# Performance work log

Hardware: AMD Instinct MI355X
Metric: run time of the kernel (lower is better)

Reference implementation:

```python
import jax, jax.numpy as jnp
import numpy as np

V, EMB, H, N, E, B = 100000, 300, 64, 20000, 160000, 4096
L, T = 2, 3  # layer_timesteps = [3, 3]


def setup_inputs() -> dict:
    key = jax.random.key(0)
    ks = jax.random.split(key, 24)
    ri = lambda k, shape, hi: jax.random.randint(k, shape, 0, hi)
    rn = lambda k, shape, s=0.05: (jax.random.normal(k, shape, dtype=jnp.float32) * s)
    emb_table = rn(ks[7], (V, EMB), 0.1).at[0].set(0.0)  # padding_idx=0 row is zeros
    return {
        'emb_ind0': ri(ks[0], (N,), V),
        'emb_ind1': ri(ks[1], (N,), V),
        'adj0': ri(ks[2], (E, 2), N),
        'adj1': ri(ks[3], (E, 2), N),
        'prop_ind0': ri(ks[4], (B,), N),
        'prop_ind1': ri(ks[5], (B,), N),
        'labels': ri(ks[6], (B,), 2),
        'emb_table': emb_table,
        'proj_W': rn(ks[8], (EMB, H)),   # emb_proj weight (stored input-major)
        'proj_b': jnp.zeros((H,), jnp.float32),
        'msg_W': rn(ks[9], (L, H, H)),   # per-layer edge-type-0 message linear
        'msg_b': jnp.zeros((L, H), jnp.float32),
        'gru_Wih': rn(ks[10], (L, 3 * H, H)),
        'gru_Whh': rn(ks[11], (L, 3 * H, H)),
        'gru_bih': jnp.zeros((L, 3 * H), jnp.float32),
        'gru_bhh': jnp.zeros((L, 3 * H), jnp.float32),
        'cla_W1': rn(ks[12], (2 * H, 16)),
        'cla_b1': jnp.zeros((16,), jnp.float32),
        'cla_W2': rn(ks[13], (16, 1)),
        'cla_b2': jnp.zeros((1,), jnp.float32),
    }


def _gru_cell(x, h, Wih, Whh, bih, bhh):
    # torch.nn.GRUCell math
    gi = x @ Wih.T + bih
    gh = h @ Whh.T + bhh
    i_r, i_z, i_n = jnp.split(gi, 3, axis=-1)
    h_r, h_z, h_n = jnp.split(gh, 3, axis=-1)
    r = jax.nn.sigmoid(i_r + h_r)
    z = jax.nn.sigmoid(i_z + h_z)
    n = jnp.tanh(i_n + r * h_n)
    return (1.0 - z) * n + z * h


def reference(emb_ind0, emb_ind1, adj0, adj1, prop_ind0, prop_ind1, labels,
              emb_table, proj_W, proj_b, msg_W, msg_b,
              gru_Wih, gru_Whh, gru_bih, gru_bhh,
              cla_W1, cla_b1, cla_W2, cla_b2):
    def ggnn(x, adj):
        src, tgt = adj[:, 0], adj[:, 1]
        h = x
        for l in range(L):              # 2 structurally distinct layers
            for _ in range(T):          # 3 timesteps each
                m = h[src] @ msg_W[l] + msg_b[l]                     # [E, H] gather + transform
                inc = jax.ops.segment_sum(m, tgt, num_segments=N)    # scatter-add messages
                h = _gru_cell(inc, h, gru_Wih[l], gru_Whh[l], gru_bih[l], gru_bhh[l])
        return h

    def branch(emb_ind, adj, prop_ind):
        ge = emb_table[emb_ind]          # embedding lookup [N, EMB]
        ge = ge @ proj_W + proj_b        # emb_proj -> [N, H]
        ge = ggnn(ge, adj)
        return ge[prop_ind]              # index_select -> [B, H]

    g0 = branch(emb_ind0, adj0, prop_ind0)
    g1 = branch(emb_ind1, adj1, prop_ind1)
    ge = jnp.concatenate([g0, g1], axis=-1)                 # match='concat' -> [B, 2H]
    hid = jax.nn.relu(ge @ cla_W1 + cla_b1)
    logits = jax.nn.sigmoid(hid @ cla_W2 + cla_b2)          # [B, 1], num_class=1 path
    p = logits.squeeze(-1)
    y = labels.astype(p.dtype)
    eps = 1e-7  # mirrors torch BCELoss log-clamping
    loss = -jnp.mean(y * jnp.log(jnp.clip(p, eps, 1.0))
                     + (1.0 - y) * jnp.log(jnp.clip(1.0 - p, eps, 1.0)))
    return logits, loss
```

## Files before the change

### kernel.cpp

```cpp
#include <hip/hip_runtime.h>
#include <hip/hip_bf16.h>

typedef unsigned short u16;
typedef __attribute__((ext_vector_type(8))) short s16x8;
typedef __attribute__((ext_vector_type(4))) float f32x4;

#define NN 20000
#define HH 64
#define EMBD 300
#define EE 160000
#define BB 4096
#define NODES 40000

#define PROJM_REP 7

#define OFF_PROJB 0
#define OFF_MSGB  64
#define OFF_BIH   192
#define OFF_BHH   576
#define OFF_CW1T  960
#define OFF_CB1   3008
#define OFF_CW2   3024
#define OFF_CB2   3040
#define PARAM_SZ  3072

#define PB_WIH   0
#define PB_WHH   24576
#define PB_WMT   49152
#define PB_PROJT 57344
#define PB_SZ    77824

#define APAD 344

#define ZCNT (16 + 2 * (NN + 1))

__device__ __forceinline__ float b2f(u16 u) {
    union { unsigned int i; float f; } v; v.i = ((unsigned int)u) << 16; return v.f;
}
__device__ __forceinline__ u16 f2b(float f) {
    union { float f; unsigned int u; } v; v.f = f;
    unsigned int u = v.u;
    return (u16)((u + 0x7FFFu + ((u >> 16) & 1u)) >> 16);
}
__device__ __forceinline__ float ldf(const void* p, long long i, int isbf) {
    return isbf ? b2f(((const u16*)p)[i]) : ((const float*)p)[i];
}
__device__ __forceinline__ u16 ldb(const void* p, long long i, int isbf) {
    return isbf ? ((const u16*)p)[i] : f2b(((const float*)p)[i]);
}
__device__ __forceinline__ void stf(void* p, long long i, int isbf, float v) {
    if (isbf) ((u16*)p)[i] = f2b(v);
    else      ((float*)p)[i] = v;
}

__device__ __forceinline__ int sniff_inline(const u16* probe, int tid)
{
    u16 x = probe[2 * (tid & 63)];
    unsigned int e = (x >> 7) & 0xFF;
    unsigned long long m = __ballot(e >= 105 && e <= 127);
    return (__popcll(m) >= 48) ? 1 : 0;
}

__global__ __launch_bounds__(256) void conv_kernel(
    const void* projW, const void* projb, const void* msgW, const void* msgb,
    const void* wih, const void* whh, const void* bih, const void* bhh,
    const void* cw1, const void* cb1, const void* cw2, const void* cb2,
    float* P, u16* PB, int* zbase)
{
    int tid = threadIdx.x;
    int isbf = sniff_inline((const u16*)projW, tid);
    int i = blockIdx.x * 256 + tid;

    if (i < ZCNT) zbase[i] = 0;

    if (i < 64)    P[OFF_PROJB + i] = ldf(projb, i, isbf);
    if (i < 128)   P[OFF_MSGB + i]  = ldf(msgb, i, isbf);
    if (i < 384)   { P[OFF_BIH + i] = ldf(bih, i, isbf); P[OFF_BHH + i] = ldf(bhh, i, isbf); }
    if (i < 2048)  { int t = i >> 7, k = i & 127; P[OFF_CW1T + i] = ldf(cw1, (long long)k * 16 + t, isbf); }
    if (i < 16)    { P[OFF_CB1 + i] = ldf(cb1, i, isbf); P[OFF_CW2 + i] = ldf(cw2, i, isbf); }
    if (i == 0)    P[OFF_CB2] = ldf(cb2, 0, isbf);

    if (i < 24576) {
        int l = i / 12288, r = i - l * 12288;
        int frag = r >> 9, rr = r & 511, lane = rr >> 3, e = rr & 7;
        int jt = frag >> 1, kt = frag & 1;
        int srow = jt * 16 + (lane & 15);
        int sk = kt * 32 + ((lane >> 4) << 3) + e;
        long long si = (long long)l * 12288 + srow * 64 + sk;
        PB[PB_WIH + i] = ldb(wih, si, isbf);
        PB[PB_WHH + i] = ldb(whh, si, isbf);
    }
    if (i < 8192) {
        int l = i >> 12, r = i & 4095;
        int frag = r >> 9, rr = r & 511, lane = rr >> 3, e = rr & 7;
        int jt = frag >> 1, kt = frag & 1;
        int srow = jt * 16 + (lane & 15);
        int sk = kt * 32 + ((lane >> 4) << 3) + e;
        PB[PB_WMT + i] = ldb(msgW, (long long)l * 4096 + sk * 64 + srow, isbf);
    }
    if (i < 20480) {
        int frag = i >> 9, rr = i & 511, lane = rr >> 3, e = rr & 7;
        int jt = frag / 10, kt = frag - jt * 10;
        int srow = jt * 16 + (lane & 15);
        int sk = kt * 32 + ((lane >> 4) << 3) + e;
        PB[PB_PROJT + i] = (sk < 300) ? ldb(projW, (long long)sk * 64 + srow, isbf) : (u16)0;
    }
}

__global__ __launch_bounds__(256) void hist_kernel(const int* __restrict__ adj0,
                                                   const int* __restrict__ adj1, int* off)
{
    int e = blockIdx.x * 256 + threadIdx.x;
    if (e >= 2 * EE) return;
    int b = e / EE, le = e - b * EE;
    const int* adj = b ? adj1 : adj0;
    int tgt = adj[2 * le + 1];
    atomicAdd(&off[b * (NN + 1) + tgt + 1], 1);
}

__global__ __launch_bounds__(1024) void scan_kernel(int* off, int* cursor)
{
    int b = blockIdx.x;
    int* o = off + (size_t)b * (NN + 1);
    int* cur = cursor + (size_t)b * NN;
    __shared__ int wsum[16];
    __shared__ int wscan[16];
    int tid = threadIdx.x, wv = tid >> 6, lane = tid & 63;

    int vpre[20];
    #pragma unroll
    for (int c = 0; c < 20; ++c) {
        int i = c * 1024 + tid;
        vpre[c] = (i < NN) ? o[i + 1] : 0;
    }

    int base = 0;
    #pragma unroll 1
    for (int c = 0; c < 20; ++c) {
        int i = c * 1024 + tid;
        int v = vpre[c];
        int orig = v;
        #pragma unroll
        for (int d = 1; d < 64; d <<= 1) {
            int t = __shfl_up(v, d);
            if (lane >= d) v += t;
        }
        if (lane == 63) wsum[wv] = v;
        __syncthreads();
        if (tid < 16) {
            int w = wsum[tid];
            #pragma unroll
            for (int d = 1; d < 16; d <<= 1) {
                int t = __shfl_up(w, d, 16);
                if (tid >= d) w += t;
            }
            wscan[tid] = w;
        }
        __syncthreads();
        int woff = (wv == 0) ? 0 : wscan[wv - 1];
        int excl = base + woff + v - orig;
        if (i < NN) { o[i] = excl; cur[i] = excl; }
        base += wscan[15];
    }
    if (tid == 0) o[NN] = base;
}

__global__ __launch_bounds__(256) void scatter_kernel(const int* __restrict__ adj0,
                                                      const int* __restrict__ adj1,
                                                      int* cursor, int* esrc)
{
    int e = blockIdx.x * 256 + threadIdx.x;
    if (e >= 2 * EE) return;
    int b = e / EE, le = e - b * EE;
    const int* adj = b ? adj1 : adj0;
    int src = adj[2 * le + 0];
    int tgt = adj[2 * le + 1];
    int pos = atomicAdd(&cursor[b * NN + tgt], 1);
    esrc[(size_t)b * EE + pos] = src;
}

__global__ __launch_bounds__(256) void projm_kernel(const void* emb,
                                                    const int* __restrict__ i0,
                                                    const int* __restrict__ i1,
                                                    const float* __restrict__ P,
                                                    const u16* __restrict__ PB,
                                                    u16* __restrict__ h,
                                                    const u16* __restrict__ probe)
{
    __shared__ u16 sA[64 * APAD];
    int tid = threadIdx.x;
    int isbf = sniff_inline(probe, tid);
    int node0 = blockIdx.x * 64;

    #pragma unroll 1
    for (int rep = 0; rep < PROJM_REP; ++rep) {
        {
            int r = tid >> 2, sub = tid & 3;
            int n = node0 + r;
            int b = n >= NN;
            int ln = n - b * NN;
            int idx = b ? i1[ln] : i0[ln];
            if (isbf) {
                const ushort4* src = (const ushort4*)((const u16*)emb + (size_t)idx * EMBD);
                ushort4* dst = (ushort4*)(sA + r * APAD);
                for (int c = sub; c < 75; c += 4) dst[c] = src[c];
                if (sub == 0) {
                    ushort4 z = {0, 0, 0, 0};
                    for (int c = 75; c < 80; ++c) dst[c] = z;
                }
            } else {
                const float4* src = (const float4*)((const float*)emb + (size_t)idx * EMBD);
                ushort4* dst = (ushort4*)(sA + r * APAD);
                for (int c = sub; c < 75; c += 4) {
                    float4 f = src[c];
                    ushort4 o4 = { f2b(f.x), f2b(f.y), f2b(f.z), f2b(f.w) };
                    dst[c] = o4;
                }
                if (sub == 0) {
                    ushort4 z = {0, 0, 0, 0};
                    for (int c = 75; c < 80; ++c) dst[c] = z;
                }
            }
        }

        int wv = tid >> 6, lane = tid & 63, quad = lane >> 4, cn = lane & 15;
        int m0 = wv * 16;
        f32x4 acc[4];
        #pragma unroll
        for (int j = 0; j < 4; ++j) {
            float bb = P[OFF_PROJB + j * 16 + cn];
            acc[j] = {bb, bb, bb, bb};
        }
        #pragma unroll
        for (int kt = 0; kt < 10; ++kt) {
            s16x8 a = *(const s16x8*)&sA[(m0 + cn) * APAD + kt * 32 + quad * 8];
            #pragma unroll
            for (int j = 0; j < 4; ++j) {
                s16x8 bfr = *(const s16x8*)&PB[PB_PROJT + (j * 10 + kt) * 512 + lane * 8];
                acc[j] = __builtin_amdgcn_mfma_f32_16x16x32_bf16(a, bfr, acc[j], 0, 0, 0);
            }
        }
        #pragma unroll
        for (int j = 0; j < 4; ++j)
            #pragma unroll
            for (int r = 0; r < 4; ++r)
                h[(size_t)(node0 + m0 + quad * 4 + r) * 64 + j * 16 + cn] = f2b(acc[j][r]);
    }
}

__global__ __launch_bounds__(256) void fstep_kernel(const u16* __restrict__ h_old,
                                                    u16* __restrict__ h_new,
                                                    const int* __restrict__ ioff,
                                                    const int* __restrict__ esrc,
                                                    const float* __restrict__ P,
                                                    const u16* __restrict__ PB, int l)
{
    __shared__ u16 s_S[32 * 64];
    __shared__ u16 s_h[32 * 64];
    __shared__ float s_deg[32];

    int tid = threadIdx.x;
    int bsw = blockIdx.x;
    int half = (bsw >> 2) & 1;
    int t = (bsw >> 3) * 4 + (bsw & 3);
    if (t >= 625) return;
    int node0 = half * NN + t * 32;

    {
        int team = tid >> 3, oct = tid & 7;
        int node = node0 + team;
        int br = node >= NN;
        int ln = node - br * NN;
        const int* o = ioff + (size_t)br * (NN + 1);
        int s0 = o[ln], s1 = o[ln + 1];
        const int* es = esrc + (size_t)br * EE;
        const u16* hb = h_old + (size_t)br * NN * 64;

        *(uint4*)&s_h[team * 64 + oct * 8] =
            *(const uint4*)&h_old[(size_t)node * 64 + oct * 8];
        if (oct == 0) s_deg[team] = (float)(s1 - s0);

        float acc[8];
        #pragma unroll
        for (int k = 0; k < 8; ++k) acc[k] = 0.f;

        int base = s0, rem = s1 - s0;
        while (rem > 0) {
            int cnt = rem < 8 ? rem : 8;
            int myidx = es[base + (oct < cnt ? oct : cnt - 1)];
            #pragma unroll
            for (int j = 0; j < 8; ++j) {
                int e = __shfl(myidx, j, 8);
                uint4 v = *(const uint4*)&hb[(size_t)e * 64 + oct * 8];
                float w = (j < cnt) ? 1.f : 0.f;
                #pragma unroll
                for (int p = 0; p < 4; ++p) {
                    unsigned int u = ((const unsigned int*)&v)[p];
                    union { unsigned int i; float f; } lo, hi;
                    lo.i = u << 16; hi.i = u & 0xffff0000u;
                    acc[2 * p]     += w * lo.f;
                    acc[2 * p + 1] += w * hi.f;
                }
            }
            base += cnt;
            rem -= cnt;
        }

        u16 pk[8];
        #pragma unroll
        for (int k = 0; k < 8; ++k) pk[k] = f2b(acc[k]);
        *(uint4*)&s_S[team * 64 + oct * 8] = *(const uint4*)pk;
    }
    __syncthreads();

    int wv = tid >> 6, lane = tid & 63;
    int wr = wv >> 1, wc = wv & 1;
    int m0 = wr * 16;
    int quad = lane >> 4, cn = lane & 15;
    int arow = (m0 + cn) * 64 + quad * 8;
    int fl = lane * 8;

    s16x8 aS0 = *(const s16x8*)&s_S[arow];
    s16x8 aS1 = *(const s16x8*)&s_S[arow + 32];
    s16x8 aH0 = *(const s16x8*)&s_h[arow];
    s16x8 aH1 = *(const s16x8*)&s_h[arow + 32];
    __syncthreads();

    const u16* WM = PB + PB_WMT + (size_t)l * 4096;
    #pragma unroll
    for (int jtl = 0; jtl < 2; ++jtl) {
        int jt = wc * 2 + jtl;
        float mb = P[OFF_MSGB + l * 64 + jt * 16 + cn];
        f32x4 acc;
        acc[0] = s_deg[m0 + quad * 4 + 0] * mb;
        acc[1] = s_deg[m0 + quad * 4 + 1] * mb;
        acc[2] = s_deg[m0 + quad * 4 + 2] * mb;
        acc[3] = s_deg[m0 + quad * 4 + 3] * mb;
        acc = __builtin_amdgcn_mfma_f32_16x16x32_bf16(aS0, *(const s16x8*)&WM[(jt * 2 + 0) * 512 + fl], acc, 0, 0, 0);
        acc = __builtin_amdgcn_mfma_f32_16x16x32_bf16(aS1, *(const s16x8*)&WM[(jt * 2 + 1) * 512 + fl], acc, 0, 0, 0);
        #pragma unroll
        for (int r = 0; r < 4; ++r)
            s_S[(m0 + quad * 4 + r) * 64 + jt * 16 + cn] = f2b(acc[r]);
    }
    __syncthreads();

    s16x8 aI0 = *(const s16x8*)&s_S[arow];
    s16x8 aI1 = *(const s16x8*)&s_S[arow + 32];
    __syncthreads();

    const u16* WI = PB + PB_WIH + (size_t)l * 12288;
    const u16* WH = PB + PB_WHH + (size_t)l * 12288;
    const float* bi = P + OFF_BIH + l * 192;
    const float* bh = P + OFF_BHH + l * 192;

    #pragma unroll
    for (int cl = 0; cl < 2; ++cl) {
        int jt = wc * 2 + cl;
        int j0 = jt * 16;
        float vr = bi[j0 + cn], vz = bi[64 + j0 + cn], vn = bi[128 + j0 + cn];
        float wr_ = bh[j0 + cn], wz = bh[64 + j0 + cn], wn = bh[128 + j0 + cn];
        f32x4 gr = {vr, vr, vr, vr}, gz = {vz, vz, vz, vz}, gn = {vn, vn, vn, vn};
        f32x4 hr = {wr_, wr_, wr_, wr_}, hz = {wz, wz, wz, wz}, hn = {wn, wn, wn, wn};
        int fr = (jt * 2) * 512 + fl, frz = ((4 + jt) * 2) * 512 + fl, frn = ((8 + jt) * 2) * 512 + fl;
        gr = __builtin_amdgcn_mfma_f32_16x16x32_bf16(aI0, *(const s16x8*)&WI[fr], gr, 0, 0, 0);
        gr = __builtin_amdgcn_mfma_f32_16x16x32_bf16(aI1, *(const s16x8*)&WI[fr + 512], gr, 0, 0, 0);
        gz = __builtin_amdgcn_mfma_f32_16x16x32_bf16(aI0, *(const s16x8*)&WI[frz], gz, 0, 0, 0);
        gz = __builtin_amdgcn_mfma_f32_16x16x32_bf16(aI1, *(const s16x8*)&WI[frz + 512], gz, 0, 0, 0);
        gn = __builtin_amdgcn_mfma_f32_16x16x32_bf16(aI0, *(const s16x8*)&WI[frn], gn, 0, 0, 0);
        gn = __builtin_amdgcn_mfma_f32_16x16x32_bf16(aI1, *(const s16x8*)&WI[frn + 512], gn, 0, 0, 0);
        hr = __builtin_amdgcn_mfma_f32_16x16x32_bf16(aH0, *(const s16x8*)&WH[fr], hr, 0, 0, 0);
        hr = __builtin_amdgcn_mfma_f32_16x16x32_bf16(aH1, *(const s16x8*)&WH[fr + 512], hr, 0, 0, 0);
        hz = __builtin_amdgcn_mfma_f32_16x16x32_bf16(aH0, *(const s16x8*)&WH[frz], hz, 0, 0, 0);
        hz = __builtin_amdgcn_mfma_f32_16x16x32_bf16(aH1, *(const s16x8*)&WH[frz + 512], hz, 0, 0, 0);
        hn = __builtin_amdgcn_mfma_f32_16x16x32_bf16(aH0, *(const s16x8*)&WH[frn], hn, 0, 0, 0);
        hn = __builtin_amdgcn_mfma_f32_16x16x32_bf16(aH1, *(const s16x8*)&WH[frn + 512], hn, 0, 0, 0);
        #pragma unroll
        for (int r = 0; r < 4; ++r) {
            int row = m0 + quad * 4 + r;
            float rr = 1.f / (1.f + __expf(-(gr[r] + hr[r])));
            float zz = 1.f / (1.f + __expf(-(gz[r] + hz[r])));
            float nn = tanhf(gn[r] + rr * hn[r]);
            float ho = b2f(s_h[row * 64 + j0 + cn]);
            s_S[row * 64 + j0 + cn] = f2b((1.f - zz) * nn + zz * ho);
        }
    }
    __syncthreads();

    {
        int team = tid >> 3, oct = tid & 7;
        int node = node0 + team;
        *(uint4*)&h_new[(size_t)node * 64 + oct * 8] =
            *(const uint4*)&s_S[team * 64 + oct * 8];
    }
}

__global__ __launch_bounds__(256) void cls_kernel(const u16* __restrict__ h,
                                                  const int* __restrict__ p0,
                                                  const int* __restrict__ p1,
                                                  const int* __restrict__ labels,
                                                  const float* __restrict__ P,
                                                  void* out, float* partial,
                                                  const u16* __restrict__ probe)
{
    int tid = threadIdx.x;
    int isbf = sniff_inline(probe, tid);
    int wv = tid >> 6, lane = tid & 63;
    int s = blockIdx.x * 4 + wv;
    int n0 = p0[s], n1 = p1[s];
    float f0 = b2f(h[(size_t)n0 * 64 + lane]);
    float f1 = b2f(h[(size_t)(NN + n1) * 64 + lane]);
    float z = P[OFF_CB2];
    #pragma unroll
    for (int t = 0; t < 16; ++t) {
        float part = f0 * P[OFF_CW1T + t * 128 + lane] + f1 * P[OFF_CW1T + t * 128 + 64 + lane];
        #pragma unroll
        for (int off = 32; off; off >>= 1) part += __shfl_xor(part, off);
        z += fmaxf(part + P[OFF_CB1 + t], 0.f) * P[OFF_CW2 + t];
    }
    float p = 1.f / (1.f + expf(-z));
    float y = (float)labels[s];
    const float eps = 1e-7f;
    float pc  = fminf(fmaxf(p, eps), 1.f);
    float pc1 = fminf(fmaxf(1.f - p, eps), 1.f);
    float term = y * logf(pc) + (1.f - y) * logf(pc1);
    __shared__ float red[4];
    if (lane == 0) { stf(out, s, isbf, p); red[wv] = term; }
    __syncthreads();
    if (tid == 0) partial[blockIdx.x] = red[0] + red[1] + red[2] + red[3];
}

__global__ __launch_bounds__(256) void loss_kernel(const float* __restrict__ partial,
                                                   void* out, const u16* __restrict__ probe)
{
    int tid = threadIdx.x;
    int isbf = sniff_inline(probe, tid);
    __shared__ float red[256];
    float s = 0.f;
    for (int i = tid; i < 1024; i += 256) s += partial[i];
    red[tid] = s;
    __syncthreads();
    for (int d = 128; d > 0; d >>= 1) {
        if (tid < d) red[tid] += red[tid + d];
        __syncthreads();
    }
    if (tid == 0) stf(out, BB, isbf, -red[0] / (float)BB);
}

extern "C" void kernel_launch(void* const* d_in, const int* in_sizes, int n_in,
                              void* d_out, int out_size, void* d_ws, size_t ws_size,
                              hipStream_t stream)
{
    const int* adj0   = (const int*)d_in[2];
    const int* adj1   = (const int*)d_in[3];
    const int* prop0  = (const int*)d_in[4];
    const int* prop1  = (const int*)d_in[5];
    const int* labels = (const int*)d_in[6];
    const u16* probe  = (const u16*)d_in[8];

    float* P  = (float*)d_ws + 16;
    u16* PB   = (u16*)(P + PARAM_SZ);
    u16* h0   = (u16*)(((uintptr_t)(PB + PB_SZ) + 255) & ~(uintptr_t)255);
    u16* h1   = h0 + (size_t)NODES * 64;
    float* partial = (float*)(h1 + (size_t)NODES * 64);
    int* zbase  = (int*)(partial + 1024);
    int* ioff   = zbase + 16;
    int* cursor = ioff + 2 * (NN + 1) + 62;
    int* esrc   = cursor + 2 * NN;

    conv_kernel<<<157, 256, 0, stream>>>(d_in[8], d_in[9], d_in[10], d_in[11], d_in[12], d_in[13],
                                         d_in[14], d_in[15], d_in[16], d_in[17], d_in[18], d_in[19],
                                         P, PB, zbase);
    hist_kernel<<<(2 * EE) / 256, 256, 0, stream>>>(adj0, adj1, ioff);
    scan_kernel<<<2, 1024, 0, stream>>>(ioff, cursor);
    scatter_kernel<<<(2 * EE) / 256, 256, 0, stream>>>(adj0, adj1, cursor, esrc);
    projm_kernel<<<(2 * NN) / 64, 256, 0, stream>>>(d_in[7], (const int*)d_in[0],
                                                    (const int*)d_in[1], P, PB, h0, probe);

    u16* hcur = h0;
    u16* hnext = h1;
    for (int l = 0; l < 2; ++l) {
        for (int t = 0; t < 3; ++t) {
            fstep_kernel<<<1256, 256, 0, stream>>>(hcur, hnext, ioff, esrc, P, PB, l);
            u16* tmp = hcur; hcur = hnext; hnext = tmp;
        }
    }

    cls_kernel<<<BB / 4, 256, 0, stream>>>(hcur, prop0, prop1, labels, P, d_out,
                                           partial, probe);
    loss_kernel<<<1, 256, 0, stream>>>(partial, d_out, probe);
}
```

Baseline: 450.0 us.

## Drop repeated projection loop, single-pass block scan, widen gathers, trim fstep barriers

The embedding projection kernel previously ran its gather and MFMA projection seven times over the same output; it now runs once. The CSR offset scan becomes a single pass in which each thread serially scans 20 contiguous elements, replacing a 20-iteration block scan with two barriers per iteration. The embedding row gather is reorganised to use 8 lanes per row and 16-byte loads when the row is aligned. fstep writes the message result into a separate shared buffer so two barriers can be removed. The extra shared buffer adds 4 KB of LDS per block, which could reduce occupancy.

After: 386.3 us. 1.17x faster.

```diff
diff --git a/kernel.cpp b/kernel.cpp
--- a/kernel.cpp
+++ b/kernel.cpp
@@ -11,8 +11,6 @@
 #define EE 160000
 #define BB 4096
 #define NODES 40000
-
-#define PROJM_REP 7
 
 #define OFF_PROJB 0
 #define OFF_MSGB  64
@@ -124,45 +122,48 @@
     int* o = off + (size_t)b * (NN + 1);
     int* cur = cursor + (size_t)b * NN;
     __shared__ int wsum[16];
-    __shared__ int wscan[16];
+    __shared__ int woff_s[16];
     int tid = threadIdx.x, wv = tid >> 6, lane = tid & 63;
 
-    int vpre[20];
-    #pragma unroll
-    for (int c = 0; c < 20; ++c) {
-        int i = c * 1024 + tid;
-        vpre[c] = (i < NN) ? o[i + 1] : 0;
-    }
-
-    int base = 0;
-    #pragma unroll 1
-    for (int c = 0; c < 20; ++c) {
-        int i = c * 1024 + tid;
-        int v = vpre[c];
-        int orig = v;
-        #pragma unroll
-        for (int d = 1; d < 64; d <<= 1) {
-            int t = __shfl_up(v, d);
-            if (lane >= d) v += t;
+    int base = tid * 20;
+    int v[20];
+    int tot = 0;
+    #pragma unroll
+    for (int k = 0; k < 20; ++k) {
+        int i = base + k;
+        int x = (i < NN) ? o[i + 1] : 0;
+        tot += x;
+        v[k] = tot;
+    }
+    int incl = tot;
+    #pragma unroll
+    for (int d = 1; d < 64; d <<= 1) {
+        int t = __shfl_up(incl, d);
+        if (lane >= d) incl += t;
+    }
+    if (lane == 63) wsum[wv] = incl;
+    int lane_excl = incl - tot;
+    __syncthreads();
+    if (tid < 16) {
+        int w = wsum[tid];
+        int s = w;
+        #pragma unroll
+        for (int d = 1; d < 16; d <<= 1) {
+            int t = __shfl_up(s, d, 16);
+            if (tid >= d) s += t;
         }
-        if (lane == 63) wsum[wv] = v;
-        __syncthreads();
-        if (tid < 16) {
-            int w = wsum[tid];
-            #pragma unroll
-            for (int d = 1; d < 16; d <<= 1) {
-                int t = __shfl_up(w, d, 16);
-                if (tid >= d) w += t;
-            }
-            wscan[tid] = w;
-        }
-        __syncthreads();
-        int woff = (wv == 0) ? 0 : wscan[wv - 1];
-        int excl = base + woff + v - orig;
-        if (i < NN) { o[i] = excl; cur[i] = excl; }
-        base += wscan[15];
-    }
-    if (tid == 0) o[NN] = base;
+        woff_s[tid] = s - w;
+    }
+    __syncthreads();
+    int pexcl = woff_s[wv] + lane_excl;
+    int run = pexcl;
+    #pragma unroll
+    for (int k = 0; k < 20; ++k) {
+        int i = base + k;
+        if (i < NN) { o[i] = run; cur[i] = run; }
+        run = pexcl + v[k];
+    }
+    if (tid == 1023) o[NN] = pexcl;
 }
 
 __global__ __launch_bounds__(256) void scatter_kernel(const int* __restrict__ adj0,
@@ -191,61 +192,75 @@
     int tid = threadIdx.x;
     int isbf = sniff_inline(probe, tid);
     int node0 = blockIdx.x * 64;
-
-    #pragma unroll 1
-    for (int rep = 0; rep < PROJM_REP; ++rep) {
-        {
-            int r = tid >> 2, sub = tid & 3;
+    int wv = tid >> 6, lane = tid & 63;
+
+    {
+        int oct = lane & 7;
+        int rbase = wv * 16 + (lane >> 3);
+        #pragma unroll
+        for (int rr = 0; rr < 2; ++rr) {
+            int r = rbase + rr * 8;
             int n = node0 + r;
-            int b = n >= NN;
-            int ln = n - b * NN;
-            int idx = b ? i1[ln] : i0[ln];
+            int bb2 = n >= NN;
+            int ln = n - bb2 * NN;
+            int idx = bb2 ? i1[ln] : i0[ln];
+            u16* dst = sA + r * APAD;
             if (isbf) {
-                const ushort4* src = (const ushort4*)((const u16*)emb + (size_t)idx * EMBD);
-                ushort4* dst = (ushort4*)(sA + r * APAD);
-                for (int c = sub; c < 75; c += 4) dst[c] = src[c];
-                if (sub == 0) {
+                const u16* src = (const u16*)emb + (size_t)idx * EMBD;
+                if ((idx & 1) == 0) {
+                    for (int c = oct; c < 37; c += 8)
+                        *(uint4*)(dst + c * 8) = *(const uint4*)(src + c * 8);
+                    if (oct == 7)
+                        *(uint2*)(dst + 296) = *(const uint2*)(src + 296);
+                } else {
+                    for (int c = oct; c < 75; c += 8)
+                        *(uint2*)(dst + c * 4) = *(const uint2*)(src + c * 4);
+                }
+                if (oct == 0) {
                     ushort4 z = {0, 0, 0, 0};
-                    for (int c = 75; c < 80; ++c) dst[c] = z;
+                    ushort4* d4 = (ushort4*)dst;
+                    #pragma unroll
+                    for (int c = 75; c < 80; ++c) d4[c] = z;
                 }
             } else {
                 const float4* src = (const float4*)((const float*)emb + (size_t)idx * EMBD);
-                ushort4* dst = (ushort4*)(sA + r * APAD);
-                for (int c = sub; c < 75; c += 4) {
+                for (int c = oct; c < 75; c += 8) {
                     float4 f = src[c];
                     ushort4 o4 = { f2b(f.x), f2b(f.y), f2b(f.z), f2b(f.w) };
-                    dst[c] = o4;
+                    *(ushort4*)(dst + c * 4) = o4;
                 }
-                if (sub == 0) {
+                if (oct == 0) {
                     ushort4 z = {0, 0, 0, 0};
-                    for (int c = 75; c < 80; ++c) dst[c] = z;
+                    ushort4* d4 = (ushort4*)dst;
+                    #pragma unroll
+                    for (int c = 75; c < 80; ++c) d4[c] = z;
                 }
             }
         }
-
-        int wv = tid >> 6, lane = tid & 63, quad = lane >> 4, cn = lane & 15;
-        int m0 = wv * 16;
-        f32x4 acc[4];
+    }
+
+    int quad = lane >> 4, cn = lane & 15;
+    int m0 = wv * 16;
+    f32x4 acc[4];
+    #pragma unroll
+    for (int j = 0; j < 4; ++j) {
+        float bb = P[OFF_PROJB + j * 16 + cn];
+        acc[j] = {bb, bb, bb, bb};
+    }
+    #pragma unroll
+    for (int kt = 0; kt < 10; ++kt) {
+        s16x8 a = *(const s16x8*)&sA[(m0 + cn) * APAD + kt * 32 + quad * 8];
         #pragma unroll
         for (int j = 0; j < 4; ++j) {
-            float bb = P[OFF_PROJB + j * 16 + cn];
-            acc[j] = {bb, bb, bb, bb};
+            s16x8 bfr = *(const s16x8*)&PB[PB_PROJT + (j * 10 + kt) * 512 + lane * 8];
+            acc[j] = __builtin_amdgcn_mfma_f32_16x16x32_bf16(a, bfr, acc[j], 0, 0, 0);
         }
-        #pragma unroll
-        for (int kt = 0; kt < 10; ++kt) {
-            s16x8 a = *(const s16x8*)&sA[(m0 + cn) * APAD + kt * 32 + quad * 8];
-            #pragma unroll
-            for (int j = 0; j < 4; ++j) {
-                s16x8 bfr = *(const s16x8*)&PB[PB_PROJT + (j * 10 + kt) * 512 + lane * 8];
-                acc[j] = __builtin_amdgcn_mfma_f32_16x16x32_bf16(a, bfr, acc[j], 0, 0, 0);
-            }
-        }
-        #pragma unroll
-        for (int j = 0; j < 4; ++j)
-            #pragma unroll
-            for (int r = 0; r < 4; ++r)
-                h[(size_t)(node0 + m0 + quad * 4 + r) * 64 + j * 16 + cn] = f2b(acc[j][r]);
-    }
+    }
+    #pragma unroll
+    for (int j = 0; j < 4; ++j)
+        #pragma unroll
+        for (int r = 0; r < 4; ++r)
+            h[(size_t)(node0 + m0 + quad * 4 + r) * 64 + j * 16 + cn] = f2b(acc[j][r]);
 }
 
 __global__ __launch_bounds__(256) void fstep_kernel(const u16* __restrict__ h_old,
@@ -257,6 +272,7 @@
 {
     __shared__ u16 s_S[32 * 64];
     __shared__ u16 s_h[32 * 64];
+    __shared__ u16 s_inc[32 * 64];
     __shared__ float s_deg[32];
 
     int tid = threadIdx.x;
@@ -324,7 +340,6 @@
     s16x8 aS1 = *(const s16x8*)&s_S[arow + 32];
     s16x8 aH0 = *(const s16x8*)&s_h[arow];
     s16x8 aH1 = *(const s16x8*)&s_h[arow + 32];
-    __syncthreads();
 
     const u16* WM = PB + PB_WMT + (size_t)l * 4096;
     #pragma unroll
@@ -340,14 +355,12 @@
         acc = __builtin_amdgcn_mfma_f32_16x16x32_bf16(aS1, *(const s16x8*)&WM[(jt * 2 + 1) * 512 + fl], acc, 0, 0, 0);
         #pragma unroll
         for (int r = 0; r < 4; ++r)
-            s_S[(m0 + quad * 4 + r) * 64 + jt * 16 + cn] = f2b(acc[r]);
-    }
-    __syncthreads();
-
-    s16x8 aI0 = *(const s16x8*)&s_S[arow];
-    s16x8 aI1 = *(const s16x8*)&s_S[arow + 32];
-    __syncthreads();
-
+            s_inc[(m0 + quad * 4 + r) * 64 + jt * 16 + cn] = f2b(acc[r]);
+    }
+    __syncthreads();
+
+    s16x8 aI0 = *(const s16x8*)&s_inc[arow];
+    s16x8 aI1 = *(const s16x8*)&s_inc[arow + 32];
     const u16* WI = PB + PB_WIH + (size_t)l * 12288;
     const u16* WH = PB + PB_WHH + (size_t)l * 12288;
     const float* bi = P + OFF_BIH + l * 192;
```
